# Optimization experiments

Measured on AMD Instinct MI355X. Metric: run time of the kernel, lower is better.

## Reference

```python
import jax, jax.numpy as jnp
import numpy as np

PS = 16
E = 512          # embed_dim
H = 8            # num_heads
EPS = 1e-5


def _ln(x, g, b):
    m = jnp.mean(x, axis=-1, keepdims=True)
    v = jnp.mean((x - m) ** 2, axis=-1, keepdims=True)
    return (x - m) * jax.lax.rsqrt(v + EPS) * g + b


def _mha(q_in, kv_in, in_w, in_b, out_w, out_b):
    # torch nn.MultiheadAttention: packed in_proj [3E, E], out_proj [E, E]
    Bq, Lq, _ = q_in.shape
    Lk = kv_in.shape[1]
    d = E // H
    wq, wk, wv = jnp.split(in_w, 3, axis=0)
    bq, bk, bv = jnp.split(in_b, 3, axis=0)
    q = (q_in @ wq.T + bq).reshape(Bq, Lq, H, d)
    k = (kv_in @ wk.T + bk).reshape(Bq, Lk, H, d)
    v = (kv_in @ wv.T + bv).reshape(Bq, Lk, H, d)
    scores = jnp.einsum('bqhd,bkhd->bhqk', q, k) / jnp.sqrt(jnp.float32(d))
    a = jax.nn.softmax(scores, axis=-1)
    o = jnp.einsum('bhqk,bkhd->bqhd', a, v).reshape(Bq, Lq, E)
    return o @ out_w.T + out_b


def setup_inputs() -> dict:
    key = jax.random.key(0)
    ks = jax.random.split(key, 24)
    s = 0.02
    D = 3 * PS * PS
    inp = {
        'neighbor_patches': jax.random.normal(ks[0], (8, 32, 32, 9, 3, PS, PS), jnp.float32),
        'w_pe': jax.random.normal(ks[1], (E, D), jnp.float32) * s,
        'b_pe': jnp.zeros((E,), jnp.float32),
        'pos_embed': jax.random.normal(ks[2], (1, 9, E), jnp.float32),
        'sa_in_w': jax.random.normal(ks[3], (3 * E, E), jnp.float32) * s,
        'sa_in_b': jnp.zeros((3 * E,), jnp.float32),
        'sa_out_w': jax.random.normal(ks[4], (E, E), jnp.float32) * s,
        'sa_out_b': jnp.zeros((E,), jnp.float32),
        'g1': jnp.ones((E,), jnp.float32), 'beta1': jnp.zeros((E,), jnp.float32),
        'ca_in_w': jax.random.normal(ks[5], (3 * E, E), jnp.float32) * s,
        'ca_in_b': jnp.zeros((3 * E,), jnp.float32),
        'ca_out_w': jax.random.normal(ks[6], (E, E), jnp.float32) * s,
        'ca_out_b': jnp.zeros((E,), jnp.float32),
        'g2': jnp.ones((E,), jnp.float32), 'beta2': jnp.zeros((E,), jnp.float32),
        'w1': jax.random.normal(ks[7], (4 * E, E), jnp.float32) * s,
        'b1': jnp.zeros((4 * E,), jnp.float32),
        'w2': jax.random.normal(ks[8], (E, 4 * E), jnp.float32) * s,
        'b2': jnp.zeros((E,), jnp.float32),
        'g3': jnp.ones((E,), jnp.float32), 'beta3': jnp.zeros((E,), jnp.float32),
    }
    return inp


def reference(neighbor_patches, w_pe, b_pe, pos_embed,
              sa_in_w, sa_in_b, sa_out_w, sa_out_b, g1, beta1,
              ca_in_w, ca_in_b, ca_out_w, ca_out_b, g2, beta2,
              w1, b1, w2, b2, g3, beta3):
    B, NH, NW, NN, C, ps, _ = neighbor_patches.shape
    x = neighbor_patches.reshape(B * NH * NW, NN, C * ps * ps)
    x = x @ w_pe.T + b_pe                       # [BN, 9, E]
    x = x + pos_embed
    attn = _mha(x, x, sa_in_w, sa_in_b, sa_out_w, sa_out_b)
    x = _ln(x + attn, g1, beta1)
    cq = x[:, 4:5, :]                            # center query [BN, 1, E]
    attn = _mha(cq, x, ca_in_w, ca_in_b, ca_out_w, ca_out_b)
    c = _ln(cq + attn, g2, beta2)
    ffn = jax.nn.gelu(c @ w1.T + b1, approximate=False) @ w2.T + b2
    out = _ln(c + ffn, g3, beta3)
    return out[:, 0, :].reshape(B, NH * NW, E)
```

## Files before the change

kernel.cpp:

```cpp
#include <hip/hip_runtime.h>


typedef unsigned short u16;
typedef u16   u16x8 __attribute__((ext_vector_type(8)));
typedef u16   u16x4 __attribute__((ext_vector_type(4)));
typedef __bf16 bf16x8 __attribute__((ext_vector_type(8)));
typedef __bf16 bf16x4 __attribute__((ext_vector_type(4)));
typedef float f32x4 __attribute__((ext_vector_type(4)));

static __device__ __forceinline__ u16 f2bf(float f) {
  union { float f; unsigned u; } v; v.f = f;
  unsigned r = v.u + 0x7FFFu + ((v.u >> 16) & 1u);
  return (u16)(r >> 16);
}
static __device__ __forceinline__ float bf2f(u16 u) {
  union { unsigned u; float f; } v; v.u = ((unsigned)u) << 16;
  return v.f;
}

static __device__ __forceinline__ void gld16(const void* g, void* l) {
  __builtin_amdgcn_global_load_lds(
      (__attribute__((address_space(1))) unsigned int*)(size_t)g,
      (__attribute__((address_space(3))) unsigned int*)(unsigned)(size_t)l,
      16, 0, 0);
}

static __device__ __forceinline__ int xcd_swz(int bid, int nwg) {
  int q = nwg >> 3, r = nwg & 7;
  int xcd = bid & 7, sub = bid >> 3;
  return (xcd < r ? xcd * (q + 1) : r * (q + 1) + (xcd - r) * q) + sub;
}

#define BAR   __builtin_amdgcn_s_barrier()
#define VM0   asm volatile("s_waitcnt vmcnt(0)" ::: "memory")
#define VM2   asm volatile("s_waitcnt vmcnt(2)" ::: "memory")
#define LGKM0 asm volatile("s_waitcnt lgkmcnt(0)" ::: "memory")

template<bool HAS_RES, bool HAS_GELU>
__global__ __launch_bounds__(512, 4) void gemm_t(
    const u16* __restrict__ A, int lda,
    const u16* __restrict__ W,
    const float* __restrict__ bias,
    const u16* res, int res_stride,
    u16* out,
    int M, int N, int K, int nbx)
{
  __shared__ u16 As[2][8192];
  __shared__ u16 Bs[2][4096];

  const int t    = threadIdx.x;
  const int lane = t & 63, wv = t >> 6;
  const int swz  = xcd_swz(blockIdx.x, gridDim.x);
  const int bm   = (swz / nbx) * 256, bn = (swz % nbx) * 128;
  const int wr   = wv >> 1, wc = wv & 1;

  const int srow = lane >> 2;
  const int skk  = (((lane & 3) ^ ((lane >> 3) & 3)) << 3);
  const int lr = lane & 15;
  const int rg = (((lane >> 4) ^ ((lr >> 1) & 3)) << 3);

  f32x4 acc[4][4] = {};

  auto stage = [&](int buf, int kt) {
    #pragma unroll
    for (int c = 0; c < 2; ++c) {
      int rr = wv * 32 + c * 16 + srow;
      gld16(A + (size_t)(bm + rr) * lda + kt * 32 + skk,
            &As[buf][(wv * 2 + c) * 512]);
    }
    int rb = wv * 16 + srow;
    gld16(W + (size_t)(bn + rb) * K + kt * 32 + skk, &Bs[buf][wv * 512]);
  };

  const int nkt = K >> 5;
  stage(0, 0);
  VM0; BAR;

  int cur = 0;
  for (int kt = 0; kt < nkt; ++kt) {
    const bool pf = (kt + 1 < nkt);
    if (pf) stage(cur ^ 1, kt + 1);

    bf16x8 a[4], b[4];
    #pragma unroll
    for (int m = 0; m < 4; ++m)
      a[m] = *(const bf16x8*)&As[cur][(wr * 64 + m * 16 + lr) * 32 + rg];
    #pragma unroll
    for (int n = 0; n < 4; ++n)
      b[n] = *(const bf16x8*)&Bs[cur][(wc * 64 + n * 16 + lr) * 32 + rg];
    #pragma unroll
    for (int m = 0; m < 4; ++m)
      #pragma unroll
      for (int n = 0; n < 4; ++n)
        acc[m][n] = __builtin_amdgcn_mfma_f32_16x16x32_bf16(a[m], b[n], acc[m][n], 0, 0, 0);

    if (pf) VM0;
    BAR;
    cur ^= 1;
  }

  const int lq = lane >> 4;
  #pragma unroll
  for (int m = 0; m < 4; ++m) {
    #pragma unroll
    for (int n = 0; n < 4; ++n) {
      int col = bn + wc * 64 + n * 16 + lr;
      float bv = bias[col];
      #pragma unroll
      for (int r = 0; r < 4; ++r) {
        int row = bm + wr * 64 + m * 16 + lq * 4 + r;
        float v = acc[m][n][r] + bv;
        if constexpr (HAS_RES) v += bf2f(res[(size_t)row * res_stride + col]);
        if constexpr (HAS_GELU) v = 0.5f * v * (1.f + erff(v * 0.70710678118f));
        out[(size_t)row * N + col] = f2bf(v);
      }
    }
  }
}

template<bool A_F32, bool HAS_POS, bool HAS_RES, bool HAS_GELU>
__global__ __launch_bounds__(256, 4) void gemm_k2(
    const void* Av, int lda,
    const u16* __restrict__ W,
    const float* __restrict__ bias,
    const float* __restrict__ pos,
    const u16* res, int res_stride,
    u16* out,
    int M, int N, int K, int nbx)
{
  __shared__ u16 As[2][4096];
  __shared__ u16 Bs[2][4096];

  const int t    = threadIdx.x;
  const int lane = t & 63, wv = t >> 6;
  const int swz  = xcd_swz(blockIdx.x, gridDim.x);
  const int bm   = (swz / nbx) * 128, bn = (swz % nbx) * 128;
  const int wr   = wv >> 1, wc = wv & 1;

  const int srow = lane >> 2;
  const int skk  = (((lane & 3) ^ ((lane >> 3) & 3)) << 3);
  const int lr = lane & 15;
  const int rg = (((lane >> 4) ^ ((lr >> 1) & 3)) << 3);

  f32x4 acc[4][4] = {};
  float4 areg[4];

  auto stage = [&](int buf, int kt) {
    const u16* A = (const u16*)Av;
    #pragma unroll
    for (int c = 0; c < 2; ++c) {
      int rr = (wv + 4 * c) * 16 + srow;
      gld16(A + (size_t)(bm + rr) * lda + kt * 32 + skk, &As[buf][(wv + 4 * c) * 512]);
      gld16(W + (size_t)(bn + rr) * K   + kt * 32 + skk, &Bs[buf][(wv + 4 * c) * 512]);
    }
  };
  auto stageB = [&](int buf, int kt) {
    #pragma unroll
    for (int c = 0; c < 2; ++c) {
      int rr = (wv + 4 * c) * 16 + srow;
      gld16(W + (size_t)(bn + rr) * K + kt * 32 + skk, &Bs[buf][(wv + 4 * c) * 512]);
    }
  };
  auto loadAf32 = [&](int kt) {
    const float* A = (const float*)Av;
    #pragma unroll
    for (int i = 0; i < 4; ++i) {
      int idx = i * 256 + t, r = idx >> 3, c4 = (idx & 7) * 4;
      areg[i] = *(const float4*)(A + (size_t)(bm + r) * lda + kt * 32 + c4);
    }
  };
  auto writeAf32 = [&](int buf) {
    #pragma unroll
    for (int i = 0; i < 4; ++i) {
      int idx = i * 256 + t, r = idx >> 3, c4 = (idx & 7) * 4;
      int g = (c4 >> 3) ^ ((r >> 1) & 3);
      int off = r * 32 + g * 8 + (c4 & 4);
      bf16x4 h;
      h.x = (__bf16)areg[i].x; h.y = (__bf16)areg[i].y;
      h.z = (__bf16)areg[i].z; h.w = (__bf16)areg[i].w;
      *(u16x4*)&As[buf][off] = *(u16x4*)&h;
    }
  };

  const int nkt = K >> 5;
  if constexpr (A_F32) {
    loadAf32(0); stageB(0, 0);
    VM2;  writeAf32(0);
    VM0; LGKM0; BAR;
  } else {
    stage(0, 0);
    VM0; BAR;
  }

  int cur = 0;
  for (int kt = 0; kt < nkt; ++kt) {
    const bool pf = (kt + 1 < nkt);
    if (pf) {
      if constexpr (A_F32) { loadAf32(kt + 1); stageB(cur ^ 1, kt + 1); }
      else                 { stage(cur ^ 1, kt + 1); }
    }

    bf16x8 a[4], b[4];
    #pragma unroll
    for (int m = 0; m < 4; ++m)
      a[m] = *(const bf16x8*)&As[cur][(wr * 64 + m * 16 + lr) * 32 + rg];
    #pragma unroll
    for (int n = 0; n < 4; ++n)
      b[n] = *(const bf16x8*)&Bs[cur][(wc * 64 + n * 16 + lr) * 32 + rg];
    #pragma unroll
    for (int m = 0; m < 4; ++m)
      #pragma unroll
      for (int n = 0; n < 4; ++n)
        acc[m][n] = __builtin_amdgcn_mfma_f32_16x16x32_bf16(a[m], b[n], acc[m][n], 0, 0, 0);

    if (pf) {
      if constexpr (A_F32) { VM2; writeAf32(cur ^ 1); VM0; LGKM0; }
      else                 { VM0; }
    }
    BAR;
    cur ^= 1;
  }

  const int lq = lane >> 4;
  #pragma unroll
  for (int m = 0; m < 4; ++m) {
    #pragma unroll
    for (int n = 0; n < 4; ++n) {
      int col = bn + wc * 64 + n * 16 + lr;
      float bv = bias[col];
      #pragma unroll
      for (int r = 0; r < 4; ++r) {
        int row = bm + wr * 64 + m * 16 + lq * 4 + r;
        float v = acc[m][n][r] + bv;
        if constexpr (HAS_POS) v += pos[(row % 9) * 512 + col];
        if constexpr (HAS_RES) v += bf2f(res[(size_t)row * res_stride + col]);
        if constexpr (HAS_GELU) v = 0.5f * v * (1.f + erff(v * 0.70710678118f));
        out[(size_t)row * N + col] = f2bf(v);
      }
    }
  }
}

__global__ __launch_bounds__(256) void ln_k(
    const u16* in,
    const float* __restrict__ g, const float* __restrict__ be,
    u16* out_bf, float* out_f32, int rows)
{
  int wv = threadIdx.x >> 6, lane = threadIdx.x & 63;
  int row = blockIdx.x * 4 + wv;
  if (row >= rows) return;
  const u16* p = in + (size_t)row * 512;
  u16x8 v = *(const u16x8*)&p[lane * 8];
  float x[8], s = 0.f, sq = 0.f;
  #pragma unroll
  for (int j = 0; j < 8; ++j) { x[j] = bf2f(v[j]); s += x[j]; sq += x[j] * x[j]; }
  #pragma unroll
  for (int o = 32; o > 0; o >>= 1) { s += __shfl_xor(s, o, 64); sq += __shfl_xor(sq, o, 64); }
  float mean = s * (1.f / 512.f);
  float var  = sq * (1.f / 512.f) - mean * mean;
  float rs   = rsqrtf(var + 1e-5f);
  float y[8];
  #pragma unroll
  for (int j = 0; j < 8; ++j) {
    int c = lane * 8 + j;
    y[j] = (x[j] - mean) * rs * g[c] + be[c];
  }
  if (out_bf) {
    u16x8 o8;
    #pragma unroll
    for (int j = 0; j < 8; ++j) o8[j] = f2bf(y[j]);
    *(u16x8*)&out_bf[(size_t)row * 512 + lane * 8] = o8;
  }
  if (out_f32) {
    #pragma unroll
    for (int j = 0; j < 8; ++j) out_f32[(size_t)row * 512 + lane * 8 + j] = y[j];
  }
}

__global__ __launch_bounds__(256) void sa_attn_k(const u16* __restrict__ qkv,
                                                 u16* __restrict__ out)
{
  __shared__ u16  s_qkv[9 * 1536];
  __shared__ float s_sc[8][81];
  const int s = blockIdx.x, t = threadIdx.x;
  const u16* src = qkv + (size_t)s * 9 * 1536;
  for (int i = t; i < (9 * 1536) / 8; i += 256)
    *(u16x8*)&s_qkv[i * 8] = *(const u16x8*)&src[i * 8];
  __syncthreads();

  const int h = t >> 5, sl = t & 31;
  for (int p = sl; p < 81; p += 32) {
    int qi = p / 9, ki = p % 9;
    const u16* qp = &s_qkv[qi * 1536 + h * 64];
    const u16* kp = &s_qkv[ki * 1536 + 512 + h * 64];
    float d = 0.f;
    #pragma unroll
    for (int e8 = 0; e8 < 8; ++e8) {
      u16x8 qv = *(const u16x8*)&qp[e8 * 8];
      u16x8 kv = *(const u16x8*)&kp[e8 * 8];
      #pragma unroll
      for (int j = 0; j < 8; ++j) d += bf2f(qv[j]) * bf2f(kv[j]);
    }
    s_sc[h][p] = d * 0.125f;
  }
  __syncthreads();

  if (t < 72) {
    int hh = t / 9, qi = t % 9;
    float* sc = &s_sc[hh][qi * 9];
    float mx = sc[0];
    #pragma unroll
    for (int i = 1; i < 9; ++i) mx = fmaxf(mx, sc[i]);
    float e[9], sum = 0.f;
    #pragma unroll
    for (int i = 0; i < 9; ++i) { e[i] = __expf(sc[i] - mx); sum += e[i]; }
    float inv = 1.f / sum;
    #pragma unroll
    for (int i = 0; i < 9; ++i) sc[i] = e[i] * inv;
  }
  __syncthreads();

  for (int gidx = sl; gidx < 72; gidx += 32) {
    int qi = gidx >> 3, dg = gidx & 7;
    float a[8] = {};
    #pragma unroll
    for (int ki = 0; ki < 9; ++ki) {
      float pr = s_sc[h][qi * 9 + ki];
      u16x8 vv = *(const u16x8*)&s_qkv[ki * 1536 + 1024 + h * 64 + dg * 8];
      #pragma unroll
      for (int j = 0; j < 8; ++j) a[j] += pr * bf2f(vv[j]);
    }
    u16x8 o8;
    #pragma unroll
    for (int j = 0; j < 8; ++j) o8[j] = f2bf(a[j]);
    *(u16x8*)&out[((size_t)s * 9 + qi) * 512 + h * 64 + dg * 8] = o8;
  }
}

__global__ __launch_bounds__(256) void ca_attn_k(const u16* __restrict__ q,
                                                 const u16* __restrict__ kv,
                                                 u16* __restrict__ out)
{
  __shared__ u16  s_q[512];
  __shared__ u16  s_kv[9 * 1024];
  __shared__ float s_sc[8][9];
  const int s = blockIdx.x, t = threadIdx.x;
  if (t < 64) *(u16x8*)&s_q[t * 8] = *(const u16x8*)&q[(size_t)s * 512 + t * 8];
  for (int i = t; i < (9 * 1024) / 8; i += 256)
    *(u16x8*)&s_kv[i * 8] = *(const u16x8*)&kv[(size_t)s * 9 * 1024 + i * 8];
  __syncthreads();

  if (t < 72) {
    int h = t / 9, ki = t % 9;
    const u16* qp = &s_q[h * 64];
    const u16* kp = &s_kv[ki * 1024 + h * 64];
    float d = 0.f;
    #pragma unroll
    for (int e8 = 0; e8 < 8; ++e8) {
      u16x8 qv = *(const u16x8*)&qp[e8 * 8];
      u16x8 kvv = *(const u16x8*)&kp[e8 * 8];
      #pragma unroll
      for (int j = 0; j < 8; ++j) d += bf2f(qv[j]) * bf2f(kvv[j]);
    }
    s_sc[h][ki] = d * 0.125f;
  }
  __syncthreads();

  if (t < 8) {
    float* sc = s_sc[t];
    float mx = sc[0];
    #pragma unroll
    for (int i = 1; i < 9; ++i) mx = fmaxf(mx, sc[i]);
    float e[9], sum = 0.f;
    #pragma unroll
    for (int i = 0; i < 9; ++i) { e[i] = __expf(sc[i] - mx); sum += e[i]; }
    float inv = 1.f / sum;
    #pragma unroll
    for (int i = 0; i < 9; ++i) sc[i] = e[i] * inv;
  }
  __syncthreads();

  if (t < 64) {
    int h = t >> 3, dg = t & 7;
    float a[8] = {};
    #pragma unroll
    for (int ki = 0; ki < 9; ++ki) {
      float pr = s_sc[h][ki];
      u16x8 vv = *(const u16x8*)&s_kv[ki * 1024 + 512 + h * 64 + dg * 8];
      #pragma unroll
      for (int j = 0; j < 8; ++j) a[j] += pr * bf2f(vv[j]);
    }
    u16x8 o8;
    #pragma unroll
    for (int j = 0; j < 8; ++j) o8[j] = f2bf(a[j]);
    *(u16x8*)&out[(size_t)s * 512 + h * 64 + dg * 8] = o8;
  }
}

__global__ __launch_bounds__(256) void wcvt_k(
    const float* s0, const float* s1, const float* s2, const float* s3,
    const float* s4, const float* s5, const float* s6, u16* dst)
{
  int b = blockIdx.x;
  const float* sp; long base, segStart;
  if      (b < 384)  { sp = s0; base = 0;       segStart = 0;    }
  else if (b < 1152) { sp = s1; base = 393216;  segStart = 384;  }
  else if (b < 1408) { sp = s2; base = 1179648; segStart = 1152; }
  else if (b < 2176) { sp = s3; base = 1441792; segStart = 1408; }
  else if (b < 2432) { sp = s4; base = 2228224; segStart = 2176; }
  else if (b < 3456) { sp = s5; base = 2490368; segStart = 2432; }
  else               { sp = s6; base = 3538944; segStart = 3456; }
  long loc = ((long)b - segStart) * 1024 + (long)threadIdx.x * 4;
  float4 f = *(const float4*)(sp + loc);
  u16x4 o; o.x = f2bf(f.x); o.y = f2bf(f.y); o.z = f2bf(f.z); o.w = f2bf(f.w);
  *(u16x4*)&dst[base + loc] = o;
}

extern "C" void kernel_launch(void* const* d_in, const int* in_sizes, int n_in,
                              void* d_out, int out_size, void* d_ws, size_t ws_size,
                              hipStream_t stream)
{
  const float* patches  = (const float*)d_in[0];
  const float* w_pe     = (const float*)d_in[1];
  const float* b_pe     = (const float*)d_in[2];
  const float* pos      = (const float*)d_in[3];
  const float* sa_in_w  = (const float*)d_in[4];
  const float* sa_in_b  = (const float*)d_in[5];
  const float* sa_out_w = (const float*)d_in[6];
  const float* sa_out_b = (const float*)d_in[7];
  const float* g1       = (const float*)d_in[8];
  const float* beta1    = (const float*)d_in[9];
  const float* ca_in_w  = (const float*)d_in[10];
  const float* ca_in_b  = (const float*)d_in[11];
  const float* ca_out_w = (const float*)d_in[12];
  const float* ca_out_b = (const float*)d_in[13];
  const float* g2       = (const float*)d_in[14];
  const float* beta2    = (const float*)d_in[15];
  const float* w1       = (const float*)d_in[16];
  const float* b1       = (const float*)d_in[17];
  const float* w2       = (const float*)d_in[18];
  const float* b2       = (const float*)d_in[19];
  const float* g3       = (const float*)d_in[20];
  const float* beta3    = (const float*)d_in[21];
  float* out = (float*)d_out;

  char* base = (char*)d_ws;
  u16* wbf        = (u16*)base;
  u16* w_pe_bf    = wbf;
  u16* sa_in_bf   = wbf + 393216;
  u16* sa_out_bf  = wbf + 1179648;
  u16* ca_in_bf   = wbf + 1441792;
  u16* ca_out_bf  = wbf + 2228224;
  u16* w1_bf      = wbf + 2490368;
  u16* w2_bf      = wbf + 3538944;
  u16* x_bf  = (u16*)(base + 9175040ull);
  u16* qkv   = (u16*)(base + 84672512ull);
  u16* sattn = (u16*)(base + 311164928ull);
  u16* q_bf  = (u16*)(base + 386662400ull);
  u16* cattn = (u16*)(base + 395051008ull);
  u16* csum  = (u16*)(base + 403439616ull);
  u16* h_bf  = (u16*)(base + 411828224ull);
  u16* osum  = (u16*)(base + 445382656ull);

  wcvt_k<<<4480, 256, 0, stream>>>(w_pe, sa_in_w, sa_out_w, ca_in_w,
                                   ca_out_w, w1, w2, wbf);

  gemm_k2<true, true, false, false><<<2304, 256, 0, stream>>>(
      patches, 768, w_pe_bf, b_pe, pos, nullptr, 0, x_bf, 73728, 512, 768, 4);
  gemm_t<false, false><<<3456, 512, 0, stream>>>(
      x_bf, 512, sa_in_bf, sa_in_b, nullptr, 0, qkv, 73728, 1536, 512, 12);
  sa_attn_k<<<8192, 256, 0, stream>>>(qkv, sattn);
  gemm_t<true, false><<<1152, 512, 0, stream>>>(
      sattn, 512, sa_out_bf, sa_out_b, x_bf, 512, x_bf, 73728, 512, 512, 4);
  ln_k<<<73728 / 4, 256, 0, stream>>>(x_bf, g1, beta1, x_bf, nullptr, 73728);
  gemm_k2<false, false, false, false><<<256, 256, 0, stream>>>(
      x_bf + 2048, 4608, ca_in_bf, ca_in_b, nullptr, nullptr, 0, q_bf, 8192, 512, 512, 4);
  gemm_t<false, false><<<2304, 512, 0, stream>>>(
      x_bf, 512, ca_in_bf + 262144, ca_in_b + 512, nullptr, 0, qkv, 73728, 1024, 512, 8);
  ca_attn_k<<<8192, 256, 0, stream>>>(q_bf, qkv, cattn);
  gemm_k2<false, false, true, false><<<256, 256, 0, stream>>>(
      cattn, 512, ca_out_bf, ca_out_b, nullptr, x_bf + 2048, 4608, csum, 8192, 512, 512, 4);
  ln_k<<<8192 / 4, 256, 0, stream>>>(csum, g2, beta2, csum, nullptr, 8192);
  gemm_t<false, true><<<512, 512, 0, stream>>>(
      csum, 512, w1_bf, b1, nullptr, 0, h_bf, 8192, 2048, 512, 16);
  gemm_k2<false, false, true, false><<<256, 256, 0, stream>>>(
      h_bf, 2048, w2_bf, b2, nullptr, csum, 512, osum, 8192, 512, 2048, 4);
  ln_k<<<8192 / 4, 256, 0, stream>>>(osum, g3, beta3, nullptr, out, 8192);
}
```

Before: 768.4 us.

## Deepen fp32 patch-embed prefetch and use smaller tiles for small GEMMs

Adds a dedicated patch-embedding GEMM that double-buffers the fp32 A operand in registers, loading two K-steps ahead so global latency overlaps the MFMA work. The small M=8192 GEMMs switch to a 64x128 tile kernel with one wave per 32 columns. This doubles their grid from 256 to 512 blocks so more CUs are busy. The cost is higher register pressure in the patch-embed kernel (occupancy hint lowered to 3) and less data reuse per tile in the small GEMMs.

```diff
diff --git a/kernel.cpp b/kernel.cpp
--- a/kernel.cpp
+++ b/kernel.cpp
@@ -33,8 +33,118 @@
 
 #define BAR   __builtin_amdgcn_s_barrier()
 #define VM0   asm volatile("s_waitcnt vmcnt(0)" ::: "memory")
-#define VM2   asm volatile("s_waitcnt vmcnt(2)" ::: "memory")
+#define VM4   asm volatile("s_waitcnt vmcnt(4)" ::: "memory")
+#define VM6   asm volatile("s_waitcnt vmcnt(6)" ::: "memory")
 #define LGKM0 asm volatile("s_waitcnt lgkmcnt(0)" ::: "memory")
+
+__global__ __launch_bounds__(256, 3) void gemm_pe(
+    const float* __restrict__ A, int lda,
+    const u16* __restrict__ W,
+    const float* __restrict__ bias,
+    const float* __restrict__ pos,
+    u16* out, int M, int N, int K, int nbx)
+{
+  __shared__ u16 As[2][4096];
+  __shared__ u16 Bs[2][4096];
+
+  const int t    = threadIdx.x;
+  const int lane = t & 63, wv = t >> 6;
+  const int swz  = xcd_swz(blockIdx.x, gridDim.x);
+  const int bm   = (swz / nbx) * 128, bn = (swz % nbx) * 128;
+  const int wr   = wv >> 1, wc = wv & 1;
+
+  const int srow = lane >> 2;
+  const int skk  = (((lane & 3) ^ ((lane >> 3) & 3)) << 3);
+  const int lr = lane & 15;
+  const int rg = (((lane >> 4) ^ ((lr >> 1) & 3)) << 3);
+
+  f32x4 acc[4][4] = {};
+  float4 areg0[4], areg1[4];
+
+  auto stageB = [&](int buf, int kt) {
+    #pragma unroll
+    for (int c = 0; c < 2; ++c) {
+      int rr = (wv + 4 * c) * 16 + srow;
+      gld16(W + (size_t)(bn + rr) * K + kt * 32 + skk, &Bs[buf][(wv + 4 * c) * 512]);
+    }
+  };
+  auto loadA = [&](float4 (&dst)[4], int kt) {
+    #pragma unroll
+    for (int i = 0; i < 4; ++i) {
+      int idx = i * 256 + t, r = idx >> 3, c4 = (idx & 7) * 4;
+      dst[i] = *(const float4*)(A + (size_t)(bm + r) * lda + kt * 32 + c4);
+    }
+  };
+  auto writeA = [&](int buf, float4 (&src)[4]) {
+    #pragma unroll
+    for (int i = 0; i < 4; ++i) {
+      int idx = i * 256 + t, r = idx >> 3, c4 = (idx & 7) * 4;
+      int g = (c4 >> 3) ^ ((r >> 1) & 3);
+      int off = r * 32 + g * 8 + (c4 & 4);
+      bf16x4 h;
+      h.x = (__bf16)src[i].x; h.y = (__bf16)src[i].y;
+      h.z = (__bf16)src[i].z; h.w = (__bf16)src[i].w;
+      *(u16x4*)&As[buf][off] = *(u16x4*)&h;
+    }
+  };
+  auto mfma_on = [&](int cur) {
+    bf16x8 a[4], b[4];
+    #pragma unroll
+    for (int m = 0; m < 4; ++m)
+      a[m] = *(const bf16x8*)&As[cur][(wr * 64 + m * 16 + lr) * 32 + rg];
+    #pragma unroll
+    for (int n = 0; n < 4; ++n)
+      b[n] = *(const bf16x8*)&Bs[cur][(wc * 64 + n * 16 + lr) * 32 + rg];
+    #pragma unroll
+    for (int m = 0; m < 4; ++m)
+      #pragma unroll
+      for (int n = 0; n < 4; ++n)
+        acc[m][n] = __builtin_amdgcn_mfma_f32_16x16x32_bf16(a[m], b[n], acc[m][n], 0, 0, 0);
+  };
+
+  const int nkt = K >> 5;
+  loadA(areg0, 0);
+  stageB(0, 0);
+  loadA(areg1, 1);
+  VM6;
+  writeA(0, areg0);
+  VM4;
+  LGKM0; BAR;
+
+  auto iter = [&](int kt, float4 (&wset)[4], float4 (&lset)[4]) {
+    const bool pf1 = kt + 1 < nkt, pf2 = kt + 2 < nkt;
+    const int cur = kt & 1;
+    if (pf1) {
+      VM0;
+      writeA(cur ^ 1, wset);
+      stageB(cur ^ 1, kt + 1);
+    }
+    if (pf2) loadA(lset, kt + 2);
+    mfma_on(cur);
+    if (pf1) { if (pf2) { VM4; } else { VM0; } }
+    LGKM0; BAR;
+  };
+  for (int kt = 0; kt < nkt; kt += 2) {
+    iter(kt,     areg1, areg0);
+    iter(kt + 1, areg0, areg1);
+  }
+
+  const int lq = lane >> 4;
+  #pragma unroll
+  for (int m = 0; m < 4; ++m) {
+    #pragma unroll
+    for (int n = 0; n < 4; ++n) {
+      int col = bn + wc * 64 + n * 16 + lr;
+      float bv = bias[col];
+      #pragma unroll
+      for (int r = 0; r < 4; ++r) {
+        int row = bm + wr * 64 + m * 16 + lq * 4 + r;
+        float v = acc[m][n][r] + bv + pos[(row % 9) * 512 + col];
+        out[(size_t)row * N + col] = f2bf(v);
+      }
+    }
+  }
+}
 
 template<bool HAS_RES, bool HAS_GELU>
 __global__ __launch_bounds__(512, 4) void gemm_t(
@@ -118,105 +228,64 @@
   }
 }
 
-template<bool A_F32, bool HAS_POS, bool HAS_RES, bool HAS_GELU>
-__global__ __launch_bounds__(256, 4) void gemm_k2(
-    const void* Av, int lda,
+template<bool HAS_RES, bool HAS_GELU>
+__global__ __launch_bounds__(256, 6) void gemm_s(
+    const u16* __restrict__ A, int lda,
     const u16* __restrict__ W,
     const float* __restrict__ bias,
-    const float* __restrict__ pos,
     const u16* res, int res_stride,
     u16* out,
     int M, int N, int K, int nbx)
 {
-  __shared__ u16 As[2][4096];
+  __shared__ u16 As[2][2048];
   __shared__ u16 Bs[2][4096];
 
   const int t    = threadIdx.x;
   const int lane = t & 63, wv = t >> 6;
   const int swz  = xcd_swz(blockIdx.x, gridDim.x);
-  const int bm   = (swz / nbx) * 128, bn = (swz % nbx) * 128;
-  const int wr   = wv >> 1, wc = wv & 1;
+  const int bm   = (swz / nbx) * 64, bn = (swz % nbx) * 128;
+  const int wc   = wv;
 
   const int srow = lane >> 2;
   const int skk  = (((lane & 3) ^ ((lane >> 3) & 3)) << 3);
   const int lr = lane & 15;
   const int rg = (((lane >> 4) ^ ((lr >> 1) & 3)) << 3);
 
-  f32x4 acc[4][4] = {};
-  float4 areg[4];
+  f32x4 acc[4][2] = {};
 
   auto stage = [&](int buf, int kt) {
-    const u16* A = (const u16*)Av;
-    #pragma unroll
-    for (int c = 0; c < 2; ++c) {
-      int rr = (wv + 4 * c) * 16 + srow;
-      gld16(A + (size_t)(bm + rr) * lda + kt * 32 + skk, &As[buf][(wv + 4 * c) * 512]);
-      gld16(W + (size_t)(bn + rr) * K   + kt * 32 + skk, &Bs[buf][(wv + 4 * c) * 512]);
-    }
-  };
-  auto stageB = [&](int buf, int kt) {
+    gld16(A + (size_t)(bm + wv * 16 + srow) * lda + kt * 32 + skk,
+          &As[buf][wv * 512]);
     #pragma unroll
     for (int c = 0; c < 2; ++c) {
       int rr = (wv + 4 * c) * 16 + srow;
       gld16(W + (size_t)(bn + rr) * K + kt * 32 + skk, &Bs[buf][(wv + 4 * c) * 512]);
     }
   };
-  auto loadAf32 = [&](int kt) {
-    const float* A = (const float*)Av;
-    #pragma unroll
-    for (int i = 0; i < 4; ++i) {
-      int idx = i * 256 + t, r = idx >> 3, c4 = (idx & 7) * 4;
-      areg[i] = *(const float4*)(A + (size_t)(bm + r) * lda + kt * 32 + c4);
-    }
-  };
-  auto writeAf32 = [&](int buf) {
-    #pragma unroll
-    for (int i = 0; i < 4; ++i) {
-      int idx = i * 256 + t, r = idx >> 3, c4 = (idx & 7) * 4;
-      int g = (c4 >> 3) ^ ((r >> 1) & 3);
-      int off = r * 32 + g * 8 + (c4 & 4);
-      bf16x4 h;
-      h.x = (__bf16)areg[i].x; h.y = (__bf16)areg[i].y;
-      h.z = (__bf16)areg[i].z; h.w = (__bf16)areg[i].w;
-      *(u16x4*)&As[buf][off] = *(u16x4*)&h;
-    }
-  };
 
   const int nkt = K >> 5;
-  if constexpr (A_F32) {
-    loadAf32(0); stageB(0, 0);
-    VM2;  writeAf32(0);
-    VM0; LGKM0; BAR;
-  } else {
-    stage(0, 0);
-    VM0; BAR;
-  }
+  stage(0, 0);
+  VM0; BAR;
 
   int cur = 0;
   for (int kt = 0; kt < nkt; ++kt) {
     const bool pf = (kt + 1 < nkt);
-    if (pf) {
-      if constexpr (A_F32) { loadAf32(kt + 1); stageB(cur ^ 1, kt + 1); }
-      else                 { stage(cur ^ 1, kt + 1); }
-    }
-
-    bf16x8 a[4], b[4];
+    if (pf) stage(cur ^ 1, kt + 1);
+
+    bf16x8 a[4], b[2];
     #pragma unroll
     for (int m = 0; m < 4; ++m)
-      a[m] = *(const bf16x8*)&As[cur][(wr * 64 + m * 16 + lr) * 32 + rg];
-    #pragma unroll
-    for (int n = 0; n < 4; ++n)
-      b[n] = *(const bf16x8*)&Bs[cur][(wc * 64 + n * 16 + lr) * 32 + rg];
+      a[m] = *(const bf16x8*)&As[cur][(m * 16 + lr) * 32 + rg];
+    #pragma unroll
+    for (int n = 0; n < 2; ++n)
+      b[n] = *(const bf16x8*)&Bs[cur][(wc * 32 + n * 16 + lr) * 32 + rg];
     #pragma unroll
     for (int m = 0; m < 4; ++m)
       #pragma unroll
-      for (int n = 0; n < 4; ++n)
+      for (int n = 0; n < 2; ++n)
         acc[m][n] = __builtin_amdgcn_mfma_f32_16x16x32_bf16(a[m], b[n], acc[m][n], 0, 0, 0);
 
-    if (pf) {
-      if constexpr (A_F32) { VM2; writeAf32(cur ^ 1); VM0; LGKM0; }
-      else                 { VM0; }
-    }
+    if (pf) VM0;
     BAR;
     cur ^= 1;
   }
@@ -225,14 +294,13 @@
   #pragma unroll
   for (int m = 0; m < 4; ++m) {
     #pragma unroll
-    for (int n = 0; n < 4; ++n) {
-      int col = bn + wc * 64 + n * 16 + lr;
+    for (int n = 0; n < 2; ++n) {
+      int col = bn + wc * 32 + n * 16 + lr;
       float bv = bias[col];
       #pragma unroll
       for (int r = 0; r < 4; ++r) {
-        int row = bm + wr * 64 + m * 16 + lq * 4 + r;
+        int row = bm + m * 16 + lq * 4 + r;
         float v = acc[m][n][r] + bv;
-        if constexpr (HAS_POS) v += pos[(row % 9) * 512 + col];
         if constexpr (HAS_RES) v += bf2f(res[(size_t)row * res_stride + col]);
         if constexpr (HAS_GELU) v = 0.5f * v * (1.f + erff(v * 0.70710678118f));
         out[(size_t)row * N + col] = f2bf(v);
@@ -465,25 +533,25 @@
   wcvt_k<<<4480, 256, 0, stream>>>(w_pe, sa_in_w, sa_out_w, ca_in_w,
                                    ca_out_w, w1, w2, wbf);
 
-  gemm_k2<true, true, false, false><<<2304, 256, 0, stream>>>(
-      patches, 768, w_pe_bf, b_pe, pos, nullptr, 0, x_bf, 73728, 512, 768, 4);
+  gemm_pe<<<2304, 256, 0, stream>>>(
+      patches, 768, w_pe_bf, b_pe, pos, x_bf, 73728, 512, 768, 4);
   gemm_t<false, false><<<3456, 512, 0, stream>>>(
       x_bf, 512, sa_in_bf, sa_in_b, nullptr, 0, qkv, 73728, 1536, 512, 12);
   sa_attn_k<<<8192, 256, 0, stream>>>(qkv, sattn);
   gemm_t<true, false><<<1152, 512, 0, stream>>>(
       sattn, 512, sa_out_bf, sa_out_b, x_bf, 512, x_bf, 73728, 512, 512, 4);
   ln_k<<<73728 / 4, 256, 0, stream>>>(x_bf, g1, beta1, x_bf, nullptr, 73728);
-  gemm_k2<false, false, false, false><<<256, 256, 0, stream>>>(
-      x_bf + 2048, 4608, ca_in_bf, ca_in_b, nullptr, nullptr, 0, q_bf, 8192, 512, 512, 4);
+  gemm_s<false, false><<<512, 256, 0, stream>>>(
+      x_bf + 2048, 4608, ca_in_bf, ca_in_b, nullptr, 0, q_bf, 8192, 512, 512, 4);
   gemm_t<false, false><<<2304, 512, 0, stream>>>(
       x_bf, 512, ca_in_bf + 262144, ca_in_b + 512, nullptr, 0, qkv, 73728, 1024, 512, 8);
   ca_attn_k<<<8192, 256, 0, stream>>>(q_bf, qkv, cattn);
-  gemm_k2<false, false, true, false><<<256, 256, 0, stream>>>(
-      cattn, 512, ca_out_bf, ca_out_b, nullptr, x_bf + 2048, 4608, csum, 8192, 512, 512, 4);
+  gemm_s<true, false><<<512, 256, 0, stream>>>(
+      cattn, 512, ca_out_bf, ca_out_b, x_bf + 2048, 4608, csum, 8192, 512, 512, 4);
   ln_k<<<8192 / 4, 256, 0, stream>>>(csum, g2, beta2, csum, nullptr, 8192);
   gemm_t<false, true><<<512, 512, 0, stream>>>(
       csum, 512, w1_bf, b1, nullptr, 0, h_bf, 8192, 2048, 512, 16);
-  gemm_k2<false, false, true, false><<<256, 256, 0, stream>>>(
-      h_bf, 2048, w2_bf, b2, nullptr, csum, 512, osum, 8192, 512, 2048, 4);
+  gemm_s<true, false><<<512, 256, 0, stream>>>(
+      h_bf, 2048, w2_bf, b2, csum, 512, osum, 8192, 512, 2048, 4);
   ln_k<<<8192 / 4, 256, 0, stream>>>(osum, g3, beta3, nullptr, out, 8192);
 }
```

Result: no change. 753.4 us, median of 2 (-2.0%).

## Pre-convert patches to bf16 and use smaller-tile GEMM for small-M layers

Applied to the files above, without the earlier changes.

Adds a separate kernel that converts the fp32 patch input to bf16, so the patch-embed GEMM can reuse the 256x128 async-load GEMM with a position-add epilogue instead of the register-staged fp32 path. Replaces the 128x128 gemm_k2 used for the 8192-row cross-attention and FFN projections with a 64x128 tile kernel that launches twice as many blocks, which should fill more of the GPU on these small problems. The cost is an extra full write and read of the roughly 113 MB bf16 patch buffer, plus less operand reuse per tile in the small GEMMs.

```diff
diff --git a/kernel.cpp b/kernel.cpp
--- a/kernel.cpp
+++ b/kernel.cpp
@@ -5,7 +5,6 @@
 typedef u16   u16x8 __attribute__((ext_vector_type(8)));
 typedef u16   u16x4 __attribute__((ext_vector_type(4)));
 typedef __bf16 bf16x8 __attribute__((ext_vector_type(8)));
-typedef __bf16 bf16x4 __attribute__((ext_vector_type(4)));
 typedef float f32x4 __attribute__((ext_vector_type(4)));
 
 static __device__ __forceinline__ u16 f2bf(float f) {
@@ -33,11 +32,93 @@
 
 #define BAR   __builtin_amdgcn_s_barrier()
 #define VM0   asm volatile("s_waitcnt vmcnt(0)" ::: "memory")
-#define VM2   asm volatile("s_waitcnt vmcnt(2)" ::: "memory")
-#define LGKM0 asm volatile("s_waitcnt lgkmcnt(0)" ::: "memory")
+
+template<bool HAS_POS, bool HAS_RES, bool HAS_GELU>
+__global__ __launch_bounds__(512, 4) void gemm_t(
+    const u16* __restrict__ A, int lda,
+    const u16* __restrict__ W,
+    const float* __restrict__ bias,
+    const float* __restrict__ pos,
+    const u16* res, int res_stride,
+    u16* out,
+    int M, int N, int K, int nbx)
+{
+  __shared__ u16 As[2][8192];
+  __shared__ u16 Bs[2][4096];
+
+  const int t    = threadIdx.x;
+  const int lane = t & 63, wv = t >> 6;
+  const int swz  = xcd_swz(blockIdx.x, gridDim.x);
+  const int bm   = (swz / nbx) * 256, bn = (swz % nbx) * 128;
+  const int wr   = wv >> 1, wc = wv & 1;
+
+  const int srow = lane >> 2;
+  const int skk  = (((lane & 3) ^ ((lane >> 3) & 3)) << 3);
+  const int lr = lane & 15;
+  const int rg = (((lane >> 4) ^ ((lr >> 1) & 3)) << 3);
+
+  f32x4 acc[4][4] = {};
+
+  auto stage = [&](int buf, int kt) {
+    #pragma unroll
+    for (int c = 0; c < 2; ++c) {
+      int rr = wv * 32 + c * 16 + srow;
+      gld16(A + (size_t)(bm + rr) * lda + kt * 32 + skk,
+            &As[buf][(wv * 2 + c) * 512]);
+    }
+    int rb = wv * 16 + srow;
+    gld16(W + (size_t)(bn + rb) * K + kt * 32 + skk, &Bs[buf][wv * 512]);
+  };
+
+  const int nkt = K >> 5;
+  stage(0, 0);
+  VM0; BAR;
+
+  int cur = 0;
+  for (int kt = 0; kt < nkt; ++kt) {
+    const bool pf = (kt + 1 < nkt);
+    if (pf) stage(cur ^ 1, kt + 1);
+
+    bf16x8 a[4], b[4];
+    #pragma unroll
+    for (int m = 0; m < 4; ++m)
+      a[m] = *(const bf16x8*)&As[cur][(wr * 64 + m * 16 + lr) * 32 + rg];
+    #pragma unroll
+    for (int n = 0; n < 4; ++n)
+      b[n] = *(const bf16x8*)&Bs[cur][(wc * 64 + n * 16 + lr) * 32 + rg];
+    #pragma unroll
+    for (int m = 0; m < 4; ++m)
+      #pragma unroll
+      for (int n = 0; n < 4; ++n)
+        acc[m][n] = __builtin_amdgcn_mfma_f32_16x16x32_bf16(a[m], b[n], acc[m][n], 0, 0, 0);
+
+    if (pf) VM0;
+    BAR;
+    cur ^= 1;
+  }
+
+  const int lq = lane >> 4;
+  #pragma unroll
+  for (int m = 0; m < 4; ++m) {
+    #pragma unroll
+    for (int n = 0; n < 4; ++n) {
+      int col = bn + wc * 64 + n * 16 + lr;
+      float bv = bias[col];
+      #pragma unroll
+      for (int r = 0; r < 4; ++r) {
+        int row = bm + wr * 64 + m * 16 + lq * 4 + r;
+        float v = acc[m][n][r] + bv;
+        if constexpr (HAS_POS) v += pos[(row % 9) * 512 + col];
+        if constexpr (HAS_RES) v += bf2f(res[(size_t)row * res_stride + col]);
+        if constexpr (HAS_GELU) v = 0.5f * v * (1.f + erff(v * 0.70710678118f));
+        out[(size_t)row * N + col] = f2bf(v);
+      }
+    }
+  }
+}
 
 template<bool HAS_RES, bool HAS_GELU>
-__global__ __launch_bounds__(512, 4) void gemm_t(
+__global__ __launch_bounds__(256, 6) void gemm_s(
     const u16* __restrict__ A, int lda,
     const u16* __restrict__ W,
     const float* __restrict__ bias,
@@ -45,31 +126,30 @@
     u16* out,
     int M, int N, int K, int nbx)
 {
-  __shared__ u16 As[2][8192];
+  __shared__ u16 As[2][2048];
   __shared__ u16 Bs[2][4096];
 
   const int t    = threadIdx.x;
   const int lane = t & 63, wv = t >> 6;
   const int swz  = xcd_swz(blockIdx.x, gridDim.x);
-  const int bm   = (swz / nbx) * 256, bn = (swz % nbx) * 128;
-  const int wr   = wv >> 1, wc = wv & 1;
+  const int bm   = (swz / nbx) * 64, bn = (swz % nbx) * 128;
+  const int wc   = wv;
 
   const int srow = lane >> 2;
   const int skk  = (((lane & 3) ^ ((lane >> 3) & 3)) << 3);
   const int lr = lane & 15;
   const int rg = (((lane >> 4) ^ ((lr >> 1) & 3)) << 3);
 
-  f32x4 acc[4][4] = {};
+  f32x4 acc[4][2] = {};
 
   auto stage = [&](int buf, int kt) {
+    gld16(A + (size_t)(bm + wv * 16 + srow) * lda + kt * 32 + skk,
+          &As[buf][wv * 512]);
     #pragma unroll
     for (int c = 0; c < 2; ++c) {
-      int rr = wv * 32 + c * 16 + srow;
-      gld16(A + (size_t)(bm + rr) * lda + kt * 32 + skk,
-            &As[buf][(wv * 2 + c) * 512]);
-    }
-    int rb = wv * 16 + srow;
-    gld16(W + (size_t)(bn + rb) * K + kt * 32 + skk, &Bs[buf][wv * 512]);
+      int rr = (wv + 4 * c) * 16 + srow;
+      gld16(W + (size_t)(bn + rr) * K + kt * 32 + skk, &Bs[buf][(wv + 4 * c) * 512]);
+    }
   };
 
   const int nkt = K >> 5;
@@ -81,17 +161,17 @@
     const bool pf = (kt + 1 < nkt);
     if (pf) stage(cur ^ 1, kt + 1);
 
-    bf16x8 a[4], b[4];
+    bf16x8 a[4], b[2];
     #pragma unroll
     for (int m = 0; m < 4; ++m)
-      a[m] = *(const bf16x8*)&As[cur][(wr * 64 + m * 16 + lr) * 32 + rg];
-    #pragma unroll
-    for (int n = 0; n < 4; ++n)
-      b[n] = *(const bf16x8*)&Bs[cur][(wc * 64 + n * 16 + lr) * 32 + rg];
+      a[m] = *(const bf16x8*)&As[cur][(m * 16 + lr) * 32 + rg];
+    #pragma unroll
+    for (int n = 0; n < 2; ++n)
+      b[n] = *(const bf16x8*)&Bs[cur][(wc * 32 + n * 16 + lr) * 32 + rg];
     #pragma unroll
     for (int m = 0; m < 4; ++m)
       #pragma unroll
-      for (int n = 0; n < 4; ++n)
+      for (int n = 0; n < 2; ++n)
         acc[m][n] = __builtin_amdgcn_mfma_f32_16x16x32_bf16(a[m], b[n], acc[m][n], 0, 0, 0);
 
     if (pf) VM0;
@@ -103,136 +183,13 @@
   #pragma unroll
   for (int m = 0; m < 4; ++m) {
     #pragma unroll
-    for (int n = 0; n < 4; ++n) {
-      int col = bn + wc * 64 + n * 16 + lr;
+    for (int n = 0; n < 2; ++n) {
+      int col = bn + wc * 32 + n * 16 + lr;
       float bv = bias[col];
       #pragma unroll
       for (int r = 0; r < 4; ++r) {
-        int row = bm + wr * 64 + m * 16 + lq * 4 + r;
+        int row = bm + m * 16 + lq * 4 + r;
         float v = acc[m][n][r] + bv;
-        if constexpr (HAS_RES) v += bf2f(res[(size_t)row * res_stride + col]);
-        if constexpr (HAS_GELU) v = 0.5f * v * (1.f + erff(v * 0.70710678118f));
-        out[(size_t)row * N + col] = f2bf(v);
-      }
-    }
-  }
-}
-
-template<bool A_F32, bool HAS_POS, bool HAS_RES, bool HAS_GELU>
-__global__ __launch_bounds__(256, 4) void gemm_k2(
-    const void* Av, int lda,
-    const u16* __restrict__ W,
-    const float* __restrict__ bias,
-    const float* __restrict__ pos,
-    const u16* res, int res_stride,
-    u16* out,
-    int M, int N, int K, int nbx)
-{
-  __shared__ u16 As[2][4096];
-  __shared__ u16 Bs[2][4096];
-
-  const int t    = threadIdx.x;
-  const int lane = t & 63, wv = t >> 6;
-  const int swz  = xcd_swz(blockIdx.x, gridDim.x);
-  const int bm   = (swz / nbx) * 128, bn = (swz % nbx) * 128;
-  const int wr   = wv >> 1, wc = wv & 1;
-
-  const int srow = lane >> 2;
-  const int skk  = (((lane & 3) ^ ((lane >> 3) & 3)) << 3);
-  const int lr = lane & 15;
-  const int rg = (((lane >> 4) ^ ((lr >> 1) & 3)) << 3);
-
-  f32x4 acc[4][4] = {};
-  float4 areg[4];
-
-  auto stage = [&](int buf, int kt) {
-    const u16* A = (const u16*)Av;
-    #pragma unroll
-    for (int c = 0; c < 2; ++c) {
-      int rr = (wv + 4 * c) * 16 + srow;
-      gld16(A + (size_t)(bm + rr) * lda + kt * 32 + skk, &As[buf][(wv + 4 * c) * 512]);
-      gld16(W + (size_t)(bn + rr) * K   + kt * 32 + skk, &Bs[buf][(wv + 4 * c) * 512]);
-    }
-  };
-  auto stageB = [&](int buf, int kt) {
-    #pragma unroll
-    for (int c = 0; c < 2; ++c) {
-      int rr = (wv + 4 * c) * 16 + srow;
-      gld16(W + (size_t)(bn + rr) * K + kt * 32 + skk, &Bs[buf][(wv + 4 * c) * 512]);
-    }
-  };
-  auto loadAf32 = [&](int kt) {
-    const float* A = (const float*)Av;
-    #pragma unroll
-    for (int i = 0; i < 4; ++i) {
-      int idx = i * 256 + t, r = idx >> 3, c4 = (idx & 7) * 4;
-      areg[i] = *(const float4*)(A + (size_t)(bm + r) * lda + kt * 32 + c4);
-    }
-  };
-  auto writeAf32 = [&](int buf) {
-    #pragma unroll
-    for (int i = 0; i < 4; ++i) {
-      int idx = i * 256 + t, r = idx >> 3, c4 = (idx & 7) * 4;
-      int g = (c4 >> 3) ^ ((r >> 1) & 3);
-      int off = r * 32 + g * 8 + (c4 & 4);
-      bf16x4 h;
-      h.x = (__bf16)areg[i].x; h.y = (__bf16)areg[i].y;
-      h.z = (__bf16)areg[i].z; h.w = (__bf16)areg[i].w;
-      *(u16x4*)&As[buf][off] = *(u16x4*)&h;
-    }
-  };
-
-  const int nkt = K >> 5;
-  if constexpr (A_F32) {
-    loadAf32(0); stageB(0, 0);
-    VM2;  writeAf32(0);
-    VM0; LGKM0; BAR;
-  } else {
-    stage(0, 0);
-    VM0; BAR;
-  }
-
-  int cur = 0;
-  for (int kt = 0; kt < nkt; ++kt) {
-    const bool pf = (kt + 1 < nkt);
-    if (pf) {
-      if constexpr (A_F32) { loadAf32(kt + 1); stageB(cur ^ 1, kt + 1); }
-      else                 { stage(cur ^ 1, kt + 1); }
-    }
-
-    bf16x8 a[4], b[4];
-    #pragma unroll
-    for (int m = 0; m < 4; ++m)
-      a[m] = *(const bf16x8*)&As[cur][(wr * 64 + m * 16 + lr) * 32 + rg];
-    #pragma unroll
-    for (int n = 0; n < 4; ++n)
-      b[n] = *(const bf16x8*)&Bs[cur][(wc * 64 + n * 16 + lr) * 32 + rg];
-    #pragma unroll
-    for (int m = 0; m < 4; ++m)
-      #pragma unroll
-      for (int n = 0; n < 4; ++n)
-        acc[m][n] = __builtin_amdgcn_mfma_f32_16x16x32_bf16(a[m], b[n], acc[m][n], 0, 0, 0);
-
-    if (pf) {
-      if constexpr (A_F32) { VM2; writeAf32(cur ^ 1); VM0; LGKM0; }
-      else                 { VM0; }
-    }
-    BAR;
-    cur ^= 1;
-  }
-
-  const int lq = lane >> 4;
-  #pragma unroll
-  for (int m = 0; m < 4; ++m) {
-    #pragma unroll
-    for (int n = 0; n < 4; ++n) {
-      int col = bn + wc * 64 + n * 16 + lr;
-      float bv = bias[col];
-      #pragma unroll
-      for (int r = 0; r < 4; ++r) {
-        int row = bm + wr * 64 + m * 16 + lq * 4 + r;
-        float v = acc[m][n][r] + bv;
-        if constexpr (HAS_POS) v += pos[(row % 9) * 512 + col];
         if constexpr (HAS_RES) v += bf2f(res[(size_t)row * res_stride + col]);
         if constexpr (HAS_GELU) v = 0.5f * v * (1.f + erff(v * 0.70710678118f));
         out[(size_t)row * N + col] = f2bf(v);
@@ -394,6 +351,18 @@
     #pragma unroll
     for (int j = 0; j < 8; ++j) o8[j] = f2bf(a[j]);
     *(u16x8*)&out[(size_t)s * 512 + h * 64 + dg * 8] = o8;
+  }
+}
+
+__global__ __launch_bounds__(256) void cvt_k(const float* __restrict__ in,
+                                             u16* __restrict__ out, long n)
+{
+  long i = ((long)blockIdx.x * 256 + threadIdx.x) * 4;
+  long stride = (long)gridDim.x * 1024;
+  for (; i < n; i += stride) {
+    float4 f = *(const float4*)&in[i];
+    u16x4 o; o.x = f2bf(f.x); o.y = f2bf(f.y); o.z = f2bf(f.z); o.w = f2bf(f.w);
+    *(u16x4*)&out[i] = o;
   }
 }
 
@@ -455,6 +424,7 @@
   u16* w2_bf      = wbf + 3538944;
   u16* x_bf  = (u16*)(base + 9175040ull);
   u16* qkv   = (u16*)(base + 84672512ull);
+  u16* pat_bf = qkv;
   u16* sattn = (u16*)(base + 311164928ull);
   u16* q_bf  = (u16*)(base + 386662400ull);
   u16* cattn = (u16*)(base + 395051008ull);
@@ -464,26 +434,27 @@
 
   wcvt_k<<<4480, 256, 0, stream>>>(w_pe, sa_in_w, sa_out_w, ca_in_w,
                                    ca_out_w, w1, w2, wbf);
-
-  gemm_k2<true, true, false, false><<<2304, 256, 0, stream>>>(
-      patches, 768, w_pe_bf, b_pe, pos, nullptr, 0, x_bf, 73728, 512, 768, 4);
-  gemm_t<false, false><<<3456, 512, 0, stream>>>(
-      x_bf, 512, sa_in_bf, sa_in_b, nullptr, 0, qkv, 73728, 1536, 512, 12);
+  cvt_k<<<2048, 256, 0, stream>>>(patches, pat_bf, 56623104L);
+
+  gemm_t<true, false, false><<<1152, 512, 0, stream>>>(
+      pat_bf, 768, w_pe_bf, b_pe, pos, nullptr, 0, x_bf, 73728, 512, 768, 4);
+  gemm_t<false, false, false><<<3456, 512, 0, stream>>>(
+      x_bf, 512, sa_in_bf, sa_in_b, nullptr, nullptr, 0, qkv, 73728, 1536, 512, 12);
   sa_attn_k<<<8192, 256, 0, stream>>>(qkv, sattn);
-  gemm_t<true, false><<<1152, 512, 0, stream>>>(
-      sattn, 512, sa_out_bf, sa_out_b, x_bf, 512, x_bf, 73728, 512, 512, 4);
+  gemm_t<false, true, false><<<1152, 512, 0, stream>>>(
+      sattn, 512, sa_out_bf, sa_out_b, nullptr, x_bf, 512, x_bf, 73728, 512, 512, 4);
   ln_k<<<73728 / 4, 256, 0, stream>>>(x_bf, g1, beta1, x_bf, nullptr, 73728);
-  gemm_k2<false, false, false, false><<<256, 256, 0, stream>>>(
-      x_bf + 2048, 4608, ca_in_bf, ca_in_b, nullptr, nullptr, 0, q_bf, 8192, 512, 512, 4);
-  gemm_t<false, false><<<2304, 512, 0, stream>>>(
-      x_bf, 512, ca_in_bf + 262144, ca_in_b + 512, nullptr, 0, qkv, 73728, 1024, 512, 8);
+  gemm_s<false, false><<<512, 256, 0, stream>>>(
+      x_bf + 2048, 4608, ca_in_bf, ca_in_b, nullptr, 0, q_bf, 8192, 512, 512, 4);
+  gemm_t<false, false, false><<<2304, 512, 0, stream>>>(
+      x_bf, 512, ca_in_bf + 262144, ca_in_b + 512, nullptr, nullptr, 0, qkv, 73728, 1024, 512, 8);
   ca_attn_k<<<8192, 256, 0, stream>>>(q_bf, qkv, cattn);
-  gemm_k2<false, false, true, false><<<256, 256, 0, stream>>>(
-      cattn, 512, ca_out_bf, ca_out_b, nullptr, x_bf + 2048, 4608, csum, 8192, 512, 512, 4);
+  gemm_s<true, false><<<512, 256, 0, stream>>>(
+      cattn, 512, ca_out_bf, ca_out_b, x_bf + 2048, 4608, csum, 8192, 512, 512, 4);
   ln_k<<<8192 / 4, 256, 0, stream>>>(csum, g2, beta2, csum, nullptr, 8192);
-  gemm_t<false, true><<<512, 512, 0, stream>>>(
-      csum, 512, w1_bf, b1, nullptr, 0, h_bf, 8192, 2048, 512, 16);
-  gemm_k2<false, false, true, false><<<256, 256, 0, stream>>>(
-      h_bf, 2048, w2_bf, b2, nullptr, csum, 512, osum, 8192, 512, 2048, 4);
+  gemm_t<false, false, true><<<512, 512, 0, stream>>>(
+      csum, 512, w1_bf, b1, nullptr, nullptr, 0, h_bf, 8192, 2048, 512, 16);
+  gemm_s<true, false><<<512, 256, 0, stream>>>(
+      h_bf, 2048, w2_bf, b2, csum, 512, osum, 8192, 512, 2048, 4);
   ln_k<<<8192 / 4, 256, 0, stream>>>(osum, g3, beta3, nullptr, out, 8192);
 }
```

Result: no change. 776.8 us (+1.1%).
